# Kernel tuning notes

Hardware: AMD Instinct MI355X
Metric: run time of the kernel (lower is better)

Reference implementation:

```python
import jax, jax.numpy as jnp
import numpy as np

EPS = 1e-6

def setup_inputs() -> dict:
    key = jax.random.key(0)
    k1, k2 = jax.random.split(key)
    fx = jax.random.normal(k1, (16, 128, 3, 4096), dtype=jnp.float32)
    fy = jax.random.normal(k2, (16, 128, 3, 4096), dtype=jnp.float32)
    return {"fx": fx, "fy": fy, "topk": 4}


def reference(fx, fy, topk):
    # fx, fy: [b, c, d=3, n]
    fx_mean = jnp.mean(fx, axis=1)                                  # [b, d, n]
    fy_mean = jnp.mean(fy, axis=1)
    fx_par = fx_mean / (jnp.linalg.norm(fx_mean, axis=1, keepdims=True) + EPS)
    fy_par = fy_mean / (jnp.linalg.norm(fy_mean, axis=1, keepdims=True) + EPS)
    phi_x = jnp.einsum('bcdn,bdn->bnc', fx, fx_par)                 # [b, n, c]
    phi_y = jnp.einsum('bcdn,bdn->bnc', fy, fy_par)
    Sc = jax.nn.softmax(jnp.einsum('bnc,bnc->bn', phi_x, phi_y), axis=-1)  # [b, n]
    k = Sc.shape[1] // topk
    idx = jax.lax.top_k(Sc, k)[1]                                   # [b, k]
    idx4 = idx[:, None, None, :]                                    # broadcast over c, d
    fx_sel = jnp.take_along_axis(fx, idx4, axis=-1)                 # [b, c, 3, k]
    fy_sel = jnp.take_along_axis(fy, idx4, axis=-1)
    return fx_sel, fy_sel
```

## Files before the change

kernel.cpp:

```cpp
#include <hip/hip_runtime.h>

#define BB 16
#define CC 128
#define DD 3
#define NN 4096
#define KK 1024
#define BN (BB * NN)
#define CH 512

__global__ __launch_bounds__(256) void k_moments(
        const float* __restrict__ fx, const float* __restrict__ fy,
        unsigned long long* __restrict__ skey, int* __restrict__ cnt) {
    __shared__ double lds[3][15][64];
    int t = threadIdx.x;
    int p = t & 63;
    int q = t >> 6;
    int gpi = blockIdx.x * 64 + p;
    int b = gpi >> 12;
    int n = gpi & (NN - 1);

    const size_t cstride = (size_t)DD * NN;
    size_t base = ((size_t)b * CC + (size_t)q * 32) * cstride + n;

    double sx0=0,sx1=0,sx2=0, sy0=0,sy1=0,sy2=0;
    double m00=0,m01=0,m02=0, m10=0,m11=0,m12=0, m20=0,m21=0,m22=0;
    #pragma unroll 4
    for (int c = 0; c < 32; ++c) {
        size_t o = base + (size_t)c * cstride;
        double x0 = (double)fx[o], x1 = (double)fx[o + NN], x2 = (double)fx[o + 2*NN];
        double y0 = (double)fy[o], y1 = (double)fy[o + NN], y2 = (double)fy[o + 2*NN];
        sx0 += x0; sx1 += x1; sx2 += x2;
        sy0 += y0; sy1 += y1; sy2 += y2;
        m00 += x0*y0; m01 += x0*y1; m02 += x0*y2;
        m10 += x1*y0; m11 += x1*y1; m12 += x1*y2;
        m20 += x2*y0; m21 += x2*y1; m22 += x2*y2;
    }
    if (q) {
        int qq = q - 1;
        lds[qq][0][p]=sx0;  lds[qq][1][p]=sx1;  lds[qq][2][p]=sx2;
        lds[qq][3][p]=sy0;  lds[qq][4][p]=sy1;  lds[qq][5][p]=sy2;
        lds[qq][6][p]=m00;  lds[qq][7][p]=m01;  lds[qq][8][p]=m02;
        lds[qq][9][p]=m10;  lds[qq][10][p]=m11; lds[qq][11][p]=m12;
        lds[qq][12][p]=m20; lds[qq][13][p]=m21; lds[qq][14][p]=m22;
    }
    __syncthreads();
    if (!q) {
        #pragma unroll
        for (int r = 0; r < 3; ++r) {
            sx0+=lds[r][0][p];  sx1+=lds[r][1][p];  sx2+=lds[r][2][p];
            sy0+=lds[r][3][p];  sy1+=lds[r][4][p];  sy2+=lds[r][5][p];
            m00+=lds[r][6][p];  m01+=lds[r][7][p];  m02+=lds[r][8][p];
            m10+=lds[r][9][p];  m11+=lds[r][10][p]; m12+=lds[r][11][p];
            m20+=lds[r][12][p]; m21+=lds[r][13][p]; m22+=lds[r][14][p];
        }
        double mx0 = sx0*(1.0/128.0), mx1 = sx1*(1.0/128.0), mx2 = sx2*(1.0/128.0);
        double my0 = sy0*(1.0/128.0), my1 = sy1*(1.0/128.0), my2 = sy2*(1.0/128.0);
        double nx = sqrt(mx0*mx0 + mx1*mx1 + mx2*mx2) + 1e-6;
        double ny = sqrt(my0*my0 + my1*my1 + my2*my2) + 1e-6;
        double x0 = mx0/nx, x1 = mx1/nx, x2 = mx2/nx;
        double y0 = my0/ny, y1 = my1/ny, y2 = my2/ny;

        double s = x0*(y0*m00 + y1*m01 + y2*m02)
                 + x1*(y0*m10 + y1*m11 + y2*m12)
                 + x2*(y0*m20 + y1*m21 + y2*m22);

        long long bits = __double_as_longlong(s);
        unsigned long long u = (bits < 0)
            ? ~(unsigned long long)bits
            : ((unsigned long long)bits | 0x8000000000000000ULL);
        skey[gpi] = u;
        cnt[gpi] = 0;
    }
}

__global__ __launch_bounds__(256) void k_count(
        const unsigned long long* __restrict__ skey, int* __restrict__ cnt) {
    __shared__ unsigned long long tile[CH];
    int b      = blockIdx.x >> 7;
    int nchunk = (blockIdx.x >> 3) & 15;
    int mchunk = blockIdx.x & 7;
    const unsigned long long* srow = skey + b * NN;
    int m0 = mchunk * CH;
    for (int i = threadIdx.x; i < CH; i += 256)
        tile[i] = srow[m0 + i];
    __syncthreads();

    int n = nchunk * 256 + threadIdx.x;
    unsigned long long un = srow[n];
    int lim = n - m0;
    int c = 0;
    #pragma unroll 8
    for (int m = 0; m < CH; ++m) {
        unsigned long long um = tile[m];
        c += (um > un);
        c += (um == un) & (m < lim);
    }
    atomicAdd(&cnt[b * NN + n], c);
}

__global__ void k_scatter(const int* __restrict__ cnt, int* __restrict__ idx) {
    int b = blockIdx.x;
    for (int i = threadIdx.x; i < NN; i += 256) {
        int r = cnt[b * NN + i];
        if (r < KK) idx[b * KK + r] = i;
    }
}

__global__ void k_gather(const float* __restrict__ fx, const float* __restrict__ fy,
                         const int* __restrict__ idx, float* __restrict__ out) {
    int row = blockIdx.x;
    int b   = row / (CC * DD);
    const float* src = blockIdx.y ? fy : fx;
    float* dst = out + (size_t)blockIdx.y * ((size_t)BB * CC * DD * KK);
    const int* id = idx + b * KK;
    size_t sbase = (size_t)row * NN;
    size_t dbase = (size_t)row * KK;
    #pragma unroll
    for (int j = threadIdx.x; j < KK; j += 256)
        dst[dbase + j] = src[sbase + id[j]];
}

extern "C" void kernel_launch(void* const* d_in, const int* in_sizes, int n_in,
                              void* d_out, int out_size, void* d_ws, size_t ws_size,
                              hipStream_t stream) {
    const float* fx = (const float*)d_in[0];
    const float* fy = (const float*)d_in[1];
    float* out = (float*)d_out;

    unsigned long long* skey = (unsigned long long*)d_ws;
    int* cnt = (int*)(skey + BN);
    int* idx = cnt + BN;

    k_moments<<<BN / 64, 256, 0, stream>>>(fx, fy, skey, cnt);
    k_count  <<<BB * 16 * 8, 256, 0, stream>>>(skey, cnt);
    k_scatter<<<BB, 256, 0, stream>>>(cnt, idx);
    k_gather <<<dim3(BB * CC * DD, 2), 256, 0, stream>>>(fx, fy, idx, out);
}
```

Before: 328.8 us.

## Fuse scatter into gather via rank-driven writes and split channels across more warps

The separate scatter kernel is removed. The gather now streams each source row with coalesced float4 reads, reads the rank array, and writes every element whose rank is below K directly to its output position. That drops one launch and the random-index reads, but the stores become scattered. Separately, the moments kernel now handles 32 points per block, with the channels split across 8 groups of 16 instead of 4 groups of 32. This doubles the block count and shortens each thread's loop, at the cost of a two-stage LDS reduction with extra barriers. The gather now reads all of the source instead of only the selected quarter.

```diff
diff --git a/kernel.cpp b/kernel.cpp
--- a/kernel.cpp
+++ b/kernel.cpp
@@ -11,21 +11,21 @@
 __global__ __launch_bounds__(256) void k_moments(
         const float* __restrict__ fx, const float* __restrict__ fy,
         unsigned long long* __restrict__ skey, int* __restrict__ cnt) {
-    __shared__ double lds[3][15][64];
+    __shared__ double lds[4][15][32];
     int t = threadIdx.x;
-    int p = t & 63;
-    int q = t >> 6;
-    int gpi = blockIdx.x * 64 + p;
+    int p = t & 31;
+    int q = t >> 5;
+    int gpi = blockIdx.x * 32 + p;
     int b = gpi >> 12;
     int n = gpi & (NN - 1);
 
     const size_t cstride = (size_t)DD * NN;
-    size_t base = ((size_t)b * CC + (size_t)q * 32) * cstride + n;
+    size_t base = ((size_t)b * CC + (size_t)q * 16) * cstride + n;
 
     double sx0=0,sx1=0,sx2=0, sy0=0,sy1=0,sy2=0;
     double m00=0,m01=0,m02=0, m10=0,m11=0,m12=0, m20=0,m21=0,m22=0;
     #pragma unroll 4
-    for (int c = 0; c < 32; ++c) {
+    for (int c = 0; c < 16; ++c) {
         size_t o = base + (size_t)c * cstride;
         double x0 = (double)fx[o], x1 = (double)fx[o + NN], x2 = (double)fx[o + 2*NN];
         double y0 = (double)fy[o], y1 = (double)fy[o + NN], y2 = (double)fy[o + 2*NN];
@@ -35,24 +35,29 @@
         m10 += x1*y0; m11 += x1*y1; m12 += x1*y2;
         m20 += x2*y0; m21 += x2*y1; m22 += x2*y2;
     }
-    if (q) {
-        int qq = q - 1;
-        lds[qq][0][p]=sx0;  lds[qq][1][p]=sx1;  lds[qq][2][p]=sx2;
-        lds[qq][3][p]=sy0;  lds[qq][4][p]=sy1;  lds[qq][5][p]=sy2;
-        lds[qq][6][p]=m00;  lds[qq][7][p]=m01;  lds[qq][8][p]=m02;
-        lds[qq][9][p]=m10;  lds[qq][10][p]=m11; lds[qq][11][p]=m12;
-        lds[qq][12][p]=m20; lds[qq][13][p]=m21; lds[qq][14][p]=m22;
-    }
+
+    #define STORE_SLOT(s) do { \
+        lds[s][0][p]=sx0;  lds[s][1][p]=sx1;  lds[s][2][p]=sx2;  \
+        lds[s][3][p]=sy0;  lds[s][4][p]=sy1;  lds[s][5][p]=sy2;  \
+        lds[s][6][p]=m00;  lds[s][7][p]=m01;  lds[s][8][p]=m02;  \
+        lds[s][9][p]=m10;  lds[s][10][p]=m11; lds[s][11][p]=m12; \
+        lds[s][12][p]=m20; lds[s][13][p]=m21; lds[s][14][p]=m22; } while(0)
+    #define ADD_SLOT(s) do { \
+        sx0+=lds[s][0][p];  sx1+=lds[s][1][p];  sx2+=lds[s][2][p];  \
+        sy0+=lds[s][3][p];  sy1+=lds[s][4][p];  sy2+=lds[s][5][p];  \
+        m00+=lds[s][6][p];  m01+=lds[s][7][p];  m02+=lds[s][8][p];  \
+        m10+=lds[s][9][p];  m11+=lds[s][10][p]; m12+=lds[s][11][p]; \
+        m20+=lds[s][12][p]; m21+=lds[s][13][p]; m22+=lds[s][14][p]; } while(0)
+
+    if (q >= 4) STORE_SLOT(q - 4);
     __syncthreads();
-    if (!q) {
-        #pragma unroll
-        for (int r = 0; r < 3; ++r) {
-            sx0+=lds[r][0][p];  sx1+=lds[r][1][p];  sx2+=lds[r][2][p];
-            sy0+=lds[r][3][p];  sy1+=lds[r][4][p];  sy2+=lds[r][5][p];
-            m00+=lds[r][6][p];  m01+=lds[r][7][p];  m02+=lds[r][8][p];
-            m10+=lds[r][9][p];  m11+=lds[r][10][p]; m12+=lds[r][11][p];
-            m20+=lds[r][12][p]; m21+=lds[r][13][p]; m22+=lds[r][14][p];
-        }
+    if (q < 4)  ADD_SLOT(q);
+    __syncthreads();
+    if (q >= 1 && q < 4) STORE_SLOT(q - 1);
+    __syncthreads();
+    if (q == 0) {
+        ADD_SLOT(0); ADD_SLOT(1); ADD_SLOT(2);
+
         double mx0 = sx0*(1.0/128.0), mx1 = sx1*(1.0/128.0), mx2 = sx2*(1.0/128.0);
         double my0 = sy0*(1.0/128.0), my1 = sy1*(1.0/128.0), my2 = sy2*(1.0/128.0);
         double nx = sqrt(mx0*mx0 + mx1*mx1 + mx2*mx2) + 1e-6;
@@ -71,6 +76,8 @@
         skey[gpi] = u;
         cnt[gpi] = 0;
     }
+    #undef STORE_SLOT
+    #undef ADD_SLOT
 }
 
 __global__ __launch_bounds__(256) void k_count(
@@ -98,26 +105,25 @@
     atomicAdd(&cnt[b * NN + n], c);
 }
 
-__global__ void k_scatter(const int* __restrict__ cnt, int* __restrict__ idx) {
-    int b = blockIdx.x;
-    for (int i = threadIdx.x; i < NN; i += 256) {
-        int r = cnt[b * NN + i];
-        if (r < KK) idx[b * KK + r] = i;
-    }
-}
-
-__global__ void k_gather(const float* __restrict__ fx, const float* __restrict__ fy,
-                         const int* __restrict__ idx, float* __restrict__ out) {
+__global__ __launch_bounds__(256) void k_gather(
+        const float* __restrict__ fx, const float* __restrict__ fy,
+        const int* __restrict__ cnt, float* __restrict__ out) {
     int row = blockIdx.x;
     int b   = row / (CC * DD);
     const float* src = blockIdx.y ? fy : fx;
-    float* dst = out + (size_t)blockIdx.y * ((size_t)BB * CC * DD * KK);
-    const int* id = idx + b * KK;
-    size_t sbase = (size_t)row * NN;
-    size_t dbase = (size_t)row * KK;
+    float* dst = out + (size_t)blockIdx.y * ((size_t)BB * CC * DD * KK)
+                     + (size_t)row * KK;
+    const float4* s4 = (const float4*)(src + (size_t)row * NN);
+    const int4*   c4 = (const int4*)(cnt + b * NN);
     #pragma unroll
-    for (int j = threadIdx.x; j < KK; j += 256)
-        dst[dbase + j] = src[sbase + id[j]];
+    for (int i = threadIdx.x; i < NN / 4; i += 256) {
+        float4 v = s4[i];
+        int4   r = c4[i];
+        if (r.x < KK) dst[r.x] = v.x;
+        if (r.y < KK) dst[r.y] = v.y;
+        if (r.z < KK) dst[r.z] = v.z;
+        if (r.w < KK) dst[r.w] = v.w;
+    }
 }
 
 extern "C" void kernel_launch(void* const* d_in, const int* in_sizes, int n_in,
@@ -129,10 +135,8 @@
 
     unsigned long long* skey = (unsigned long long*)d_ws;
     int* cnt = (int*)(skey + BN);
-    int* idx = cnt + BN;
 
-    k_moments<<<BN / 64, 256, 0, stream>>>(fx, fy, skey, cnt);
+    k_moments<<<BN / 32, 256, 0, stream>>>(fx, fy, skey, cnt);
     k_count  <<<BB * 16 * 8, 256, 0, stream>>>(skey, cnt);
-    k_scatter<<<BB, 256, 0, stream>>>(cnt, idx);
-    k_gather <<<dim3(BB * CC * DD, 2), 256, 0, stream>>>(fx, fy, idx, out);
+    k_gather <<<dim3(BB * CC * DD, 2), 256, 0, stream>>>(fx, fy, cnt, out);
 }
```

Measured after the change: 339.7 us. +3.3%, slower.
